# Performance work log

Hardware: AMD Instinct MI355X
Metric: run time of the kernel (lower is better)

Reference implementation:

```python
import jax, jax.numpy as jnp
import numpy as np

N1, N2, N3, N4, D = 50000, 100000, 200000, 300000, 256


def setup_inputs() -> dict:
    key = jax.random.key(0)
    ks = jax.random.split(key, 10)
    feat = jax.random.normal(ks[0], (N1, D), dtype=jnp.float32) * 0.5  # scaled so level-4 products stay bounded
    c2a = jax.random.randint(ks[1], (N2,), 0, N1)
    c2b = jax.random.randint(ks[2], (N2,), 0, N1)
    c3a = jax.random.randint(ks[3], (N3,), 0, N2)
    c3b = jax.random.randint(ks[4], (N3,), 0, N2)
    c4a = jax.random.randint(ks[5], (N4,), 0, N3)
    c4b = jax.random.randint(ks[6], (N4,), 0, N3)
    W = jax.random.normal(ks[7], (D, D), dtype=jnp.float32) / jnp.sqrt(jnp.float32(D))
    b = jax.random.normal(ks[8], (D,), dtype=jnp.float32) * 0.01
    return {"feat": feat, "c2a": c2a, "c2b": c2b, "c3a": c3a, "c3b": c3b,
            "c4a": c4a, "c4b": c4b, "W": W, "b": b}


def _scatter_sum(h_parent, ca, cb, num_children):
    # each parent sends its feature to both children; children sum incoming messages
    z = jnp.zeros((num_children, h_parent.shape[1]), dtype=h_parent.dtype)
    return z.at[ca].add(h_parent).at[cb].add(h_parent)


def reference(feat, c2a, c2b, c3a, c3b, c4a, c4b, W, b):
    # upward: prod reduction over the two constituent subpaths (mailbox prod, dim=1)
    h1 = feat
    h2 = h1[c2a] * h1[c2b]            # [N2, D]
    h3 = h2[c3a] * h2[c3b]            # [N3, D]
    h4 = h3[c4a] * h3[c4b]            # [N4, D]
    # downward: sum-scatter parent -> children, h = h + h_down
    h3 = h3 + _scatter_sum(h4, c4a, c4b, h3.shape[0])
    h2 = h2 + _scatter_sum(h3, c3a, c3b, h2.shape[0])
    h1 = h1 + _scatter_sum(h2, c2a, c2b, h1.shape[0])
    # apply_nodes on n1: Linear + SiLU
    out = jax.nn.silu(h1 @ W + b)
    return out
```

## Files before the change

kernel.cpp:

```cpp
#include <hip/hip_runtime.h>
#include <cstdint>
#include <cstddef>

#define DD 256
#define DH 128
#define SCAN_BLK 256
#define SCAN_ELEMS 2048

__device__ __forceinline__ float2 mul2(float2 a, float2 b) {
    return make_float2(a.x * b.x, a.y * b.y);
}
__device__ __forceinline__ float2 add2(float2 a, float2 b) {
    return make_float2(a.x + b.x, a.y + b.y);
}
__device__ __forceinline__ float2 ldh(const float* __restrict__ base, int row, int lane) {
    return ((const float2*)(base + (size_t)row * DH))[lane];
}
__device__ __forceinline__ float2 ldf(const float* __restrict__ base, int row, int doff, int lane) {
    return ((const float2*)(base + (size_t)row * DD + doff))[lane];
}

__global__ void k_count_pairs(const int* __restrict__ ea, const int* __restrict__ eb,
                              int ne, int* __restrict__ cnt) {
    int e = blockIdx.x * blockDim.x + threadIdx.x;
    if (e >= ne) return;
    atomicAdd(&cnt[ea[e]], 1);
    atomicAdd(&cnt[eb[e]], 1);
}

__global__ void k_fill_edges(const int* __restrict__ ea, const int* __restrict__ eb,
                             int ne, int* __restrict__ cursor, int* __restrict__ ent) {
    int e = blockIdx.x * blockDim.x + threadIdx.x;
    if (e >= ne) return;
    int a = ea[e], b = eb[e];
    int pa = atomicAdd(&cursor[a], 1);
    int pb = atomicAdd(&cursor[b], 1);
    ent[pa] = e;
    ent[pb] = e;
}

__global__ void k_fill_pairs4(const int* __restrict__ c4a, const int* __restrict__ c4b,
                              const int* __restrict__ c3a, const int* __restrict__ c3b,
                              int ne, int* __restrict__ cursor, int2* __restrict__ entp) {
    int e = blockIdx.x * blockDim.x + threadIdx.x;
    if (e >= ne) return;
    int a = c4a[e], b = c4b[e];
    int2 prA = make_int2(c3a[b], c3b[b]);
    int2 prB = make_int2(c3a[a], c3b[a]);
    int pa = atomicAdd(&cursor[a], 1);
    int pb = atomicAdd(&cursor[b], 1);
    entp[pa] = prA;
    entp[pb] = prB;
}

__global__ void k_block_sums(const int* __restrict__ cnt, int n, int* __restrict__ bsum) {
    __shared__ int sdata[SCAN_BLK];
    int base = blockIdx.x * SCAN_ELEMS;
    int s = 0;
#pragma unroll
    for (int k = 0; k < 8; ++k) {
        int idx = base + threadIdx.x + k * SCAN_BLK;
        if (idx < n) s += cnt[idx];
    }
    sdata[threadIdx.x] = s;
    __syncthreads();
    for (int off = SCAN_BLK / 2; off > 0; off >>= 1) {
        if (threadIdx.x < off) sdata[threadIdx.x] += sdata[threadIdx.x + off];
        __syncthreads();
    }
    if (threadIdx.x == 0) bsum[blockIdx.x] = sdata[0];
}

__global__ void k_scan_bsums(int* __restrict__ bsum, int nb, int* __restrict__ total_out) {
    if (threadIdx.x == 0 && blockIdx.x == 0) {
        int acc = 0;
        for (int b = 0; b < nb; ++b) { int v = bsum[b]; bsum[b] = acc; acc += v; }
        *total_out = acc;
    }
}

__global__ void k_scan_final(const int* __restrict__ cnt, int n,
                             const int* __restrict__ bsum, int* __restrict__ offs) {
    __shared__ int sdata[SCAN_BLK];
    int base = blockIdx.x * SCAN_ELEMS;
    int t0 = base + threadIdx.x * 8;
    int loc[8];
    int s = 0;
#pragma unroll
    for (int k = 0; k < 8; ++k) {
        int idx = t0 + k;
        int v = (idx < n) ? cnt[idx] : 0;
        loc[k] = s;
        s += v;
    }
    sdata[threadIdx.x] = s;
    __syncthreads();
    int run = s;
    for (int off = 1; off < SCAN_BLK; off <<= 1) {
        int add = (threadIdx.x >= (unsigned)off) ? sdata[threadIdx.x - off] : 0;
        __syncthreads();
        run += add;
        sdata[threadIdx.x] = run;
        __syncthreads();
    }
    int texcl = run - s + bsum[blockIdx.x];
#pragma unroll
    for (int k = 0; k < 8; ++k) {
        int idx = t0 + k;
        if (idx < n) offs[idx] = texcl + loc[k];
    }
}

__global__ void k_flat_cnt(const int* __restrict__ offs2, const int* __restrict__ ent2,
                           const int* __restrict__ offs3, int n1, int* __restrict__ cntF) {
    int i = blockIdx.x * blockDim.x + threadIdx.x;
    if (i >= n1) return;
    int c = 0;
    int e0 = offs2[i], e1 = offs2[i + 1];
    for (int e = e0; e < e1; ++e) {
        int q = ent2[e];
        c += offs3[q + 1] - offs3[q];
    }
    cntF[i] = c;
}

__global__ void k_flat_fill(const int* __restrict__ offs2, const int* __restrict__ ent2,
                            const int* __restrict__ offs3, const int* __restrict__ ent3,
                            const int* __restrict__ offsF, int n1, int* __restrict__ entF) {
    int i = blockIdx.x * blockDim.x + threadIdx.x;
    if (i >= n1) return;
    int pos = offsF[i];
    int e0 = offs2[i], e1 = offs2[i + 1];
    for (int e = e0; e < e1; ++e) {
        int q = ent2[e];
        int f0 = offs3[q], f1 = offs3[q + 1];
        for (int f = f0; f < f1; ++f) entF[pos++] = ent3[f];
    }
}

__global__ void k_h2_half(const float* __restrict__ feat, const int* __restrict__ c2a,
                          const int* __restrict__ c2b, float* __restrict__ h2h,
                          int n2, int doff) {
    int q = blockIdx.x * 4 + (threadIdx.x >> 6);
    int lane = threadIdx.x & 63;
    if (q >= n2) return;
    float2 v = mul2(ldf(feat, c2a[q], doff, lane), ldf(feat, c2b[q], doff, lane));
    ((float2*)(h2h + (size_t)q * DH))[lane] = v;
}

__global__ void k_h3tot_half(const float* __restrict__ h2h,
                             const int* __restrict__ c3a, const int* __restrict__ c3b,
                             const int* __restrict__ offs4, const int2* __restrict__ entp,
                             float* __restrict__ h3th, int lo, int hi) {
    int j = lo + blockIdx.x * 4 + (threadIdx.x >> 6);
    int lane = threadIdx.x & 63;
    if (j >= hi) return;
    float2 own = mul2(ldh(h2h, c3a[j], lane), ldh(h2h, c3b[j], lane));
    float2 s = make_float2(0.f, 0.f);
    int e0 = offs4[j], e1 = offs4[j + 1];
    int e = e0;
    for (; e + 1 < e1; e += 2) {
        int2 p0 = entp[e], p1 = entp[e + 1];
        float2 a0 = ldh(h2h, p0.x, lane), b0 = ldh(h2h, p0.y, lane);
        float2 a1 = ldh(h2h, p1.x, lane), b1 = ldh(h2h, p1.y, lane);
        s = add2(s, add2(mul2(a0, b0), mul2(a1, b1)));
    }
    if (e < e1) {
        int2 p = entp[e];
        s = add2(s, mul2(ldh(h2h, p.x, lane), ldh(h2h, p.y, lane)));
    }
    float2 r = mul2(own, make_float2(1.f + s.x, 1.f + s.y));
    ((float2*)(h3th + (size_t)(j - lo) * DH))[lane] = r;
}

__global__ void k_h1_half(const float* __restrict__ feat, const float* __restrict__ h2h,
                          const int* __restrict__ offs2, const int* __restrict__ ent2,
                          const int* __restrict__ offsF, const int* __restrict__ entF,
                          const float* __restrict__ h3th, float* __restrict__ out,
                          int n1, int lo, int hi, int do_init, int doff) {
    int i = blockIdx.x * 4 + (threadIdx.x >> 6);
    int lane = threadIdx.x & 63;
    if (i >= n1) return;
    float2 h;
    if (do_init) {
        h = ldf(feat, i, doff, lane);
        int e0 = offs2[i], e1 = offs2[i + 1];
        int e = e0;
        for (; e + 1 < e1; e += 2) {
            int q0 = ent2[e], q1 = ent2[e + 1];
            h = add2(h, add2(ldh(h2h, q0, lane), ldh(h2h, q1, lane)));
        }
        if (e < e1) h = add2(h, ldh(h2h, ent2[e], lane));
    } else {
        h = ldf(out, i, doff, lane);
    }
    int f0 = offsF[i], f1 = offsF[i + 1];
    int f = f0;
    for (; f + 1 < f1; f += 2) {
        int j0 = entF[f], j1 = entF[f + 1];
        bool in0 = (j0 >= lo) && (j0 < hi);
        bool in1 = (j1 >= lo) && (j1 < hi);
        if (in0 && in1) {
            h = add2(h, add2(ldh(h3th, j0 - lo, lane), ldh(h3th, j1 - lo, lane)));
        } else if (in0) {
            h = add2(h, ldh(h3th, j0 - lo, lane));
        } else if (in1) {
            h = add2(h, ldh(h3th, j1 - lo, lane));
        }
    }
    if (f < f1) {
        int j0 = entF[f];
        if (j0 >= lo && j0 < hi) h = add2(h, ldh(h3th, j0 - lo, lane));
    }
    ((float2*)(out + (size_t)i * DD + doff))[lane] = h;
}

__device__ __forceinline__ float silu_f(float x) { return x / (1.0f + expf(-x)); }

__global__ __launch_bounds__(256) void k_gemm_silu(float* __restrict__ h,
                                                   const float* __restrict__ W,
                                                   const float* __restrict__ bias,
                                                   int n1) {
    __shared__ float As[32 * DD];
    const int t = threadIdx.x;
    const int row0 = blockIdx.x * 32;

    const float4* hv = (const float4*)h;
    float4* As4 = (float4*)As;
#pragma unroll
    for (int i = 0; i < 8; ++i) {
        int idx = t + i * 256;
        int r = idx >> 6, c = idx & 63;
        int gr = row0 + r;
        float4 v = make_float4(0.f, 0.f, 0.f, 0.f);
        if (gr < n1) v = hv[(size_t)gr * 64 + c];
        As4[idx] = v;
    }
    __syncthreads();

    const int rg = t >> 6;
    const int cg = t & 63;
    const float4* Wv = (const float4*)W;

    float4 acc[8];
#pragma unroll
    for (int r = 0; r < 8; ++r) acc[r] = make_float4(0.f, 0.f, 0.f, 0.f);

    for (int k = 0; k < DD; k += 4) {
        float4 a[8];
#pragma unroll
        for (int r = 0; r < 8; ++r)
            a[r] = *(const float4*)&As[(rg * 8 + r) * DD + k];
#pragma unroll
        for (int kk = 0; kk < 4; ++kk) {
            float4 w = Wv[(size_t)(k + kk) * 64 + cg];
#pragma unroll
            for (int r = 0; r < 8; ++r) {
                float av = (kk == 0) ? a[r].x : (kk == 1) ? a[r].y
                         : (kk == 2) ? a[r].z : a[r].w;
                acc[r].x += av * w.x;
                acc[r].y += av * w.y;
                acc[r].z += av * w.z;
                acc[r].w += av * w.w;
            }
        }
    }

    float4 bb = ((const float4*)bias)[cg];
    float4* ho = (float4*)h;
#pragma unroll
    for (int r = 0; r < 8; ++r) {
        int gr = row0 + rg * 8 + r;
        if (gr >= n1) continue;
        float4 x = acc[r];
        x.x = silu_f(x.x + bb.x);
        x.y = silu_f(x.y + bb.y);
        x.z = silu_f(x.z + bb.z);
        x.w = silu_f(x.w + bb.w);
        ho[(size_t)gr * 64 + cg] = x;
    }
}

static inline size_t al16(size_t x) { return (x + 15) & ~(size_t)15; }

extern "C" void kernel_launch(void* const* d_in, const int* in_sizes, int n_in,
                              void* d_out, int out_size, void* d_ws, size_t ws_size,
                              hipStream_t stream) {
    const float* feat = (const float*)d_in[0];
    const int* c2a = (const int*)d_in[1];
    const int* c2b = (const int*)d_in[2];
    const int* c3a = (const int*)d_in[3];
    const int* c3b = (const int*)d_in[4];
    const int* c4a = (const int*)d_in[5];
    const int* c4b = (const int*)d_in[6];
    const float* W = (const float*)d_in[7];
    const float* bias = (const float*)d_in[8];

    const int N1 = in_sizes[0] / DD;
    const int N2 = in_sizes[1];
    const int N3 = in_sizes[3];
    const int N4 = in_sizes[5];
    float* out = (float*)d_out;
    char* ws = (char*)d_ws;

    dim3 blk(256);
    auto rows_grid = [](int n) { return dim3((unsigned)((n + 3) / 4)); };
    auto thr_grid = [](int n) { return dim3((unsigned)((n + 255) / 256)); };

    int maxN = N1 > N2 ? N1 : N2;
    if (N3 > maxN) maxN = N3;

    size_t cnt_b   = al16((size_t)maxN * 4);
    size_t bsum_b  = al16(4096);
    size_t offs4_b = al16((size_t)(N3 + 1) * 4);
    size_t entp_b  = al16((size_t)2 * N4 * 8);
    size_t offs3_b = al16((size_t)(N2 + 1) * 4);
    size_t ent3_b  = al16((size_t)2 * N3 * 4);
    size_t offs2_b = al16((size_t)(N1 + 1) * 4);
    size_t ent2_b  = al16((size_t)2 * N2 * 4);
    size_t offsF_b = al16((size_t)(N1 + 1) * 4);
    size_t entF_b  = al16((size_t)4 * N3 * 4);
    size_t fixed_b = cnt_b + bsum_b + offs4_b + entp_b + offs3_b + ent3_b +
                     offs2_b + ent2_b + offsF_b + entF_b;
    size_t h2h_b = (size_t)N2 * DH * sizeof(float);

    char* p = ws;
    int* cnt   = (int*)p; p += cnt_b;
    int* bsum  = (int*)p; p += bsum_b;
    int* offs4 = (int*)p; p += offs4_b;
    int2* entp = (int2*)p; p += entp_b;
    int* offs3 = (int*)p; p += offs3_b;
    int* ent3  = (int*)p; p += ent3_b;
    int* offs2 = (int*)p; p += offs2_b;
    int* ent2  = (int*)p; p += ent2_b;
    int* offsF = (int*)p; p += offsF_b;
    int* entF  = (int*)p; p += entF_b;
    float* h2h = (float*)p; p += h2h_b;
    float* h3th = (float*)p;

    size_t free_b = (ws_size > fixed_b + h2h_b) ? ws_size - fixed_b - h2h_b : 0;
    int chunk_rows = (int)(free_b / ((size_t)DH * sizeof(float)));
    if (chunk_rows > N3) chunk_rows = N3;
    if (chunk_rows < 1) chunk_rows = 1;
    int C = (N3 + chunk_rows - 1) / chunk_rows;
    chunk_rows = (N3 + C - 1) / C;

    auto scan_offs = [&](int* cn, int nnode, int* offs) {
        int nb = (nnode + SCAN_ELEMS - 1) / SCAN_ELEMS;
        k_block_sums<<<dim3((unsigned)nb), dim3(SCAN_BLK), 0, stream>>>(cn, nnode, bsum);
        k_scan_bsums<<<dim3(1), dim3(64), 0, stream>>>(bsum, nb, offs + nnode);
        k_scan_final<<<dim3((unsigned)nb), dim3(SCAN_BLK), 0, stream>>>(cn, nnode, bsum, offs);
    };

    hipMemsetAsync(cnt, 0, (size_t)N3 * 4, stream);
    k_count_pairs<<<thr_grid(N4), blk, 0, stream>>>(c4a, c4b, N4, cnt);
    scan_offs(cnt, N3, offs4);
    hipMemcpyAsync(cnt, offs4, (size_t)N3 * 4, hipMemcpyDeviceToDevice, stream);
    k_fill_pairs4<<<thr_grid(N4), blk, 0, stream>>>(c4a, c4b, c3a, c3b, N4, cnt, entp);

    hipMemsetAsync(cnt, 0, (size_t)N2 * 4, stream);
    k_count_pairs<<<thr_grid(N3), blk, 0, stream>>>(c3a, c3b, N3, cnt);
    scan_offs(cnt, N2, offs3);
    hipMemcpyAsync(cnt, offs3, (size_t)N2 * 4, hipMemcpyDeviceToDevice, stream);
    k_fill_edges<<<thr_grid(N3), blk, 0, stream>>>(c3a, c3b, N3, cnt, ent3);

    hipMemsetAsync(cnt, 0, (size_t)N1 * 4, stream);
    k_count_pairs<<<thr_grid(N2), blk, 0, stream>>>(c2a, c2b, N2, cnt);
    scan_offs(cnt, N1, offs2);
    hipMemcpyAsync(cnt, offs2, (size_t)N1 * 4, hipMemcpyDeviceToDevice, stream);
    k_fill_edges<<<thr_grid(N2), blk, 0, stream>>>(c2a, c2b, N2, cnt, ent2);

    k_flat_cnt<<<thr_grid(N1), blk, 0, stream>>>(offs2, ent2, offs3, N1, cnt);
    scan_offs(cnt, N1, offsF);
    k_flat_fill<<<thr_grid(N1), blk, 0, stream>>>(offs2, ent2, offs3, ent3, offsF, N1, entF);

    for (int doff = 0; doff < DD; doff += DH) {
        k_h2_half<<<rows_grid(N2), blk, 0, stream>>>(feat, c2a, c2b, h2h, N2, doff);
        int do_init = 1;
        for (int lo = 0; lo < N3; lo += chunk_rows) {
            int hi = lo + chunk_rows;
            if (hi > N3) hi = N3;
            k_h3tot_half<<<rows_grid(hi - lo), blk, 0, stream>>>(h2h, c3a, c3b,
                                                                 offs4, entp,
                                                                 h3th, lo, hi);
            k_h1_half<<<rows_grid(N1), blk, 0, stream>>>(feat, h2h, offs2, ent2,
                                                         offsF, entF, h3th, out,
                                                         N1, lo, hi, do_init, doff);
            do_init = 0;
        }
    }

    k_gemm_silu<<<dim3((unsigned)((N1 + 31) / 32)), blk, 0, stream>>>(out, W, bias, N1);
}
```

Before: 852.8 us.

## Replace flattened two-hop scatter with staged level-2 accumulation

Removes the flattened two-hop edge list (count, scan and fill kernels) that made each level-1 node gather every grandchild h3 row directly. Instead it adds a k_m2_half kernel that accumulates h3 totals into level-2 rows, m2 = h2 + sum of incident h3. The level-1 kernel then gathers only the m2 rows of its direct children. This cuts the number of random row gathers and drops the preprocessing kernels. When the workspace can hold the full h3 buffer, a single unchunked path is used and m2 is written in place over h2h; otherwise an extra N2-sized buffer shrinks the chunk size available for h3.

```diff
diff --git a/kernel.cpp b/kernel.cpp
--- a/kernel.cpp
+++ b/kernel.cpp
@@ -108,33 +108,6 @@
     for (int k = 0; k < 8; ++k) {
         int idx = t0 + k;
         if (idx < n) offs[idx] = texcl + loc[k];
-    }
-}
-
-__global__ void k_flat_cnt(const int* __restrict__ offs2, const int* __restrict__ ent2,
-                           const int* __restrict__ offs3, int n1, int* __restrict__ cntF) {
-    int i = blockIdx.x * blockDim.x + threadIdx.x;
-    if (i >= n1) return;
-    int c = 0;
-    int e0 = offs2[i], e1 = offs2[i + 1];
-    for (int e = e0; e < e1; ++e) {
-        int q = ent2[e];
-        c += offs3[q + 1] - offs3[q];
-    }
-    cntF[i] = c;
-}
-
-__global__ void k_flat_fill(const int* __restrict__ offs2, const int* __restrict__ ent2,
-                            const int* __restrict__ offs3, const int* __restrict__ ent3,
-                            const int* __restrict__ offsF, int n1, int* __restrict__ entF) {
-    int i = blockIdx.x * blockDim.x + threadIdx.x;
-    if (i >= n1) return;
-    int pos = offsF[i];
-    int e0 = offs2[i], e1 = offs2[i + 1];
-    for (int e = e0; e < e1; ++e) {
-        int q = ent2[e];
-        int f0 = offs3[q], f1 = offs3[q + 1];
-        for (int f = f0; f < f1; ++f) entF[pos++] = ent3[f];
     }
 }
 
@@ -173,31 +146,18 @@
     ((float2*)(h3th + (size_t)(j - lo) * DH))[lane] = r;
 }
 
-__global__ void k_h1_half(const float* __restrict__ feat, const float* __restrict__ h2h,
-                          const int* __restrict__ offs2, const int* __restrict__ ent2,
-                          const int* __restrict__ offsF, const int* __restrict__ entF,
-                          const float* __restrict__ h3th, float* __restrict__ out,
-                          int n1, int lo, int hi, int do_init, int doff) {
-    int i = blockIdx.x * 4 + (threadIdx.x >> 6);
+__global__ void k_m2_half(const float* __restrict__ h2h,
+                          const int* __restrict__ offs3, const int* __restrict__ ent3,
+                          const float* __restrict__ h3th, float* __restrict__ dst,
+                          int n2, int lo, int hi, int first) {
+    int q = blockIdx.x * 4 + (threadIdx.x >> 6);
     int lane = threadIdx.x & 63;
-    if (i >= n1) return;
-    float2 h;
-    if (do_init) {
-        h = ldf(feat, i, doff, lane);
-        int e0 = offs2[i], e1 = offs2[i + 1];
-        int e = e0;
-        for (; e + 1 < e1; e += 2) {
-            int q0 = ent2[e], q1 = ent2[e + 1];
-            h = add2(h, add2(ldh(h2h, q0, lane), ldh(h2h, q1, lane)));
-        }
-        if (e < e1) h = add2(h, ldh(h2h, ent2[e], lane));
-    } else {
-        h = ldf(out, i, doff, lane);
-    }
-    int f0 = offsF[i], f1 = offsF[i + 1];
+    if (q >= n2) return;
+    float2 h = first ? ldh(h2h, q, lane) : ldh(dst, q, lane);
+    int f0 = offs3[q], f1 = offs3[q + 1];
     int f = f0;
     for (; f + 1 < f1; f += 2) {
-        int j0 = entF[f], j1 = entF[f + 1];
+        int j0 = ent3[f], j1 = ent3[f + 1];
         bool in0 = (j0 >= lo) && (j0 < hi);
         bool in1 = (j1 >= lo) && (j1 < hi);
         if (in0 && in1) {
@@ -209,9 +169,26 @@
         }
     }
     if (f < f1) {
-        int j0 = entF[f];
+        int j0 = ent3[f];
         if (j0 >= lo && j0 < hi) h = add2(h, ldh(h3th, j0 - lo, lane));
     }
+    ((float2*)(dst + (size_t)q * DH))[lane] = h;
+}
+
+__global__ void k_h1_half(const float* __restrict__ feat, const float* __restrict__ m2,
+                          const int* __restrict__ offs2, const int* __restrict__ ent2,
+                          float* __restrict__ out, int n1, int doff) {
+    int i = blockIdx.x * 4 + (threadIdx.x >> 6);
+    int lane = threadIdx.x & 63;
+    if (i >= n1) return;
+    float2 h = ldf(feat, i, doff, lane);
+    int e0 = offs2[i], e1 = offs2[i + 1];
+    int e = e0;
+    for (; e + 1 < e1; e += 2) {
+        int q0 = ent2[e], q1 = ent2[e + 1];
+        h = add2(h, add2(ldh(m2, q0, lane), ldh(m2, q1, lane)));
+    }
+    if (e < e1) h = add2(h, ldh(m2, ent2[e], lane));
     ((float2*)(out + (size_t)i * DD + doff))[lane] = h;
 }
 
@@ -318,11 +295,10 @@
     size_t ent3_b  = al16((size_t)2 * N3 * 4);
     size_t offs2_b = al16((size_t)(N1 + 1) * 4);
     size_t ent2_b  = al16((size_t)2 * N2 * 4);
-    size_t offsF_b = al16((size_t)(N1 + 1) * 4);
-    size_t entF_b  = al16((size_t)4 * N3 * 4);
     size_t fixed_b = cnt_b + bsum_b + offs4_b + entp_b + offs3_b + ent3_b +
-                     offs2_b + ent2_b + offsF_b + entF_b;
+                     offs2_b + ent2_b;
     size_t h2h_b = (size_t)N2 * DH * sizeof(float);
+    size_t h3th_full_b = (size_t)N3 * DH * sizeof(float);
 
     char* p = ws;
     int* cnt   = (int*)p; p += cnt_b;
@@ -333,17 +309,9 @@
     int* ent3  = (int*)p; p += ent3_b;
     int* offs2 = (int*)p; p += offs2_b;
     int* ent2  = (int*)p; p += ent2_b;
-    int* offsF = (int*)p; p += offsF_b;
-    int* entF  = (int*)p; p += entF_b;
     float* h2h = (float*)p; p += h2h_b;
-    float* h3th = (float*)p;
-
-    size_t free_b = (ws_size > fixed_b + h2h_b) ? ws_size - fixed_b - h2h_b : 0;
-    int chunk_rows = (int)(free_b / ((size_t)DH * sizeof(float)));
-    if (chunk_rows > N3) chunk_rows = N3;
-    if (chunk_rows < 1) chunk_rows = 1;
-    int C = (N3 + chunk_rows - 1) / chunk_rows;
-    chunk_rows = (N3 + C - 1) / C;
+
+    bool single = (ws_size >= fixed_b + h2h_b + h3th_full_b);
 
     auto scan_offs = [&](int* cn, int nnode, int* offs) {
         int nb = (nnode + SCAN_ELEMS - 1) / SCAN_ELEMS;
@@ -370,24 +338,44 @@
     hipMemcpyAsync(cnt, offs2, (size_t)N1 * 4, hipMemcpyDeviceToDevice, stream);
     k_fill_edges<<<thr_grid(N2), blk, 0, stream>>>(c2a, c2b, N2, cnt, ent2);
 
-    k_flat_cnt<<<thr_grid(N1), blk, 0, stream>>>(offs2, ent2, offs3, N1, cnt);
-    scan_offs(cnt, N1, offsF);
-    k_flat_fill<<<thr_grid(N1), blk, 0, stream>>>(offs2, ent2, offs3, ent3, offsF, N1, entF);
-
-    for (int doff = 0; doff < DD; doff += DH) {
-        k_h2_half<<<rows_grid(N2), blk, 0, stream>>>(feat, c2a, c2b, h2h, N2, doff);
-        int do_init = 1;
-        for (int lo = 0; lo < N3; lo += chunk_rows) {
-            int hi = lo + chunk_rows;
-            if (hi > N3) hi = N3;
-            k_h3tot_half<<<rows_grid(hi - lo), blk, 0, stream>>>(h2h, c3a, c3b,
-                                                                 offs4, entp,
-                                                                 h3th, lo, hi);
+    if (single) {
+        float* h3th = (float*)p;
+        for (int doff = 0; doff < DD; doff += DH) {
+            k_h2_half<<<rows_grid(N2), blk, 0, stream>>>(feat, c2a, c2b, h2h, N2, doff);
+            k_h3tot_half<<<rows_grid(N3), blk, 0, stream>>>(h2h, c3a, c3b, offs4, entp,
+                                                            h3th, 0, N3);
+            k_m2_half<<<rows_grid(N2), blk, 0, stream>>>(h2h, offs3, ent3, h3th,
+                                                         h2h, N2, 0, N3, 1);
             k_h1_half<<<rows_grid(N1), blk, 0, stream>>>(feat, h2h, offs2, ent2,
-                                                         offsF, entF, h3th, out,
-                                                         N1, lo, hi, do_init, doff);
-            do_init = 0;
+                                                         out, N1, doff);
         }
+    } else {
+        float* m2h = (float*)p;
+        char* pc = p + h2h_b;
+        float* h3th = (float*)pc;
+        size_t free_b = (ws_size > fixed_b + 2 * h2h_b) ? ws_size - fixed_b - 2 * h2h_b : 0;
+        int chunk_rows = (int)(free_b / ((size_t)DH * sizeof(float)));
+        if (chunk_rows > N3) chunk_rows = N3;
+        if (chunk_rows < 1) chunk_rows = 1;
+        int C = (N3 + chunk_rows - 1) / chunk_rows;
+        chunk_rows = (N3 + C - 1) / C;
+
+        for (int doff = 0; doff < DD; doff += DH) {
+            k_h2_half<<<rows_grid(N2), blk, 0, stream>>>(feat, c2a, c2b, h2h, N2, doff);
+            int first = 1;
+            for (int lo = 0; lo < N3; lo += chunk_rows) {
+                int hi = lo + chunk_rows;
+                if (hi > N3) hi = N3;
+                k_h3tot_half<<<rows_grid(hi - lo), blk, 0, stream>>>(h2h, c3a, c3b,
+                                                                     offs4, entp,
+                                                                     h3th, lo, hi);
+                k_m2_half<<<rows_grid(N2), blk, 0, stream>>>(h2h, offs3, ent3, h3th,
+                                                             m2h, N2, lo, hi, first);
+                first = 0;
+            }
+            k_h1_half<<<rows_grid(N1), blk, 0, stream>>>(feat, m2h, offs2, ent2,
+                                                         out, N1, doff);
+        }
     }
 
     k_gemm_silu<<<dim3((unsigned)((N1 + 31) / 32)), blk, 0, stream>>>(out, W, bias, N1);
```

After: 776.7 us. 8.9% less time.
